# Optimization experiments

Measured on AMD Instinct MI355X. Metric: run time of the kernel, lower is better.

Reference implementation:

```python
import jax, jax.numpy as jnp
import numpy as np

B, N, H, D, N_HEADS = 8, 2048, 1024, 1, 8
SCALE = H / N_HEADS  # 128.0 ; note: NOT sqrt, faithful to source


def _linear(x, w, b):
    # torch nn.Linear: y = x @ W^T + b ; w: [out, in]
    return jnp.einsum('bnh,oh->bno', x, w) + b


def setup_inputs() -> dict:
    key = jax.random.key(0)
    ks = jax.random.split(key, 18)
    s = 0.02
    inp = {
        'node_t': jax.random.normal(ks[0], (B, N, H), dtype=jnp.float32),
        'node_next': jax.random.normal(ks[1], (B, N, H), dtype=jnp.float32),
        'WQ_w': s * jax.random.normal(ks[2], (H, H), dtype=jnp.float32),
        'WQ_b': s * jax.random.normal(ks[3], (H,), dtype=jnp.float32),
        'WK_w': s * jax.random.normal(ks[4], (H, H), dtype=jnp.float32),
        'WK_b': s * jax.random.normal(ks[5], (H,), dtype=jnp.float32),
        'WV_w': s * jax.random.normal(ks[6], (H, H), dtype=jnp.float32),
        'WV_b': s * jax.random.normal(ks[7], (H,), dtype=jnp.float32),
        'WO_w': s * jax.random.normal(ks[8], (H, H), dtype=jnp.float32),
        'WO_b': s * jax.random.normal(ks[9], (H,), dtype=jnp.float32),
        'WE_w': s * jax.random.normal(ks[10], (H, H), dtype=jnp.float32),
        'WE_b': s * jax.random.normal(ks[11], (H,), dtype=jnp.float32),
        'WN_w': s * jax.random.normal(ks[12], (H, H), dtype=jnp.float32),
        'WN_b': s * jax.random.normal(ks[13], (H,), dtype=jnp.float32),
        'WA_w': s * jax.random.normal(ks[14], (D, H), dtype=jnp.float32),
        'WA_b': s * jax.random.normal(ks[15], (D,), dtype=jnp.float32),
    }
    return inp


def reference(node_t, node_next, WQ_w, WQ_b, WK_w, WK_b, WV_w, WV_b,
              WO_w, WO_b, WE_w, WE_b, WN_w, WN_b, WA_w, WA_b):
    Q = _linear(node_t, WQ_w, WQ_b)       # [B,N,H]
    K = _linear(node_next, WK_w, WK_b)    # [B,N,H]
    V = _linear(node_next, WV_w, WV_b)    # [B,N,H]
    att = jnp.einsum('bih,bkh->bik', Q, K)  # [B,N,N]
    # torch nn.Softmax() with no dim on a 3-D tensor -> legacy dim=0 (batch axis)
    att = jax.nn.softmax(att / SCALE, axis=0)
    # einsum('bnn,bnd->bnd') uses only the diagonal att[b,n,n]
    diag = jnp.einsum('bnn->bn', att)  # [B,N]
    av = diag[:, :, None] * V          # [B,N,H]
    h = jax.nn.gelu(_linear(av, WO_w, WO_b), approximate=False)  # exact erf GELU
    A_t = _linear(node_t, WE_w, WE_b) + _linear(h, WN_w, WN_b)   # [B,N,H]
    A_t = _linear(A_t, WA_w, WA_b)     # [B,N,1]
    return jnp.squeeze(A_t, axis=-1)   # [B,N]
```

## Files before the change

### kernel.cpp

```cpp
#include <hip/hip_runtime.h>
#include <cstdint>
#include <cstddef>


typedef __attribute__((ext_vector_type(8))) short bfx8;
typedef __attribute__((ext_vector_type(4))) short s16x4;
typedef __attribute__((ext_vector_type(4))) float f32x4;

#define N_SEQ 2048
#define M_TOT 16384
#define NT 16

__device__ __forceinline__ unsigned short f2bf(float f) {
  unsigned int u = __float_as_uint(f);
  return (unsigned short)((u + 0x7fffu + ((u >> 16) & 1u)) >> 16);
}
__device__ __forceinline__ float bf2f(short s) {
  return __uint_as_float(((unsigned int)(unsigned short)s) << 16);
}
__device__ __forceinline__ float gelu_exact(float g) {
  return 0.5f * g * (1.0f + erff(g * 0.70710678118654752f));
}
__device__ __forceinline__ void gload16(const void* g, void* l) {
  __builtin_amdgcn_global_load_lds(
      (const __attribute__((address_space(1))) unsigned int*)g,
      (__attribute__((address_space(3))) unsigned int*)(unsigned int)(uintptr_t)l,
      16, 0, 0);
}
__device__ __forceinline__ float dot4(float4 a, float4 b) {
  return a.x * b.x + a.y * b.y + a.z * b.z + a.w * b.w;
}

__global__ __launch_bounds__(256) void prep_w(
    const float* __restrict__ WQ, const float* __restrict__ WK,
    const float* __restrict__ WV, const float* __restrict__ WO,
    const float* __restrict__ WE, const float* __restrict__ WN,
    const float* __restrict__ wa, const float* __restrict__ bQ,
    const float* __restrict__ bK, const float* __restrict__ bV,
    const float* __restrict__ WEb, const float* __restrict__ WNb,
    const float* __restrict__ WAb,
    short* __restrict__ wqT, short* __restrict__ wkT,
    short* __restrict__ wvT, short* __restrict__ wo_bf,
    float* __restrict__ vE, float* __restrict__ vN,
    float* __restrict__ uQ, float* __restrict__ uK,
    float* __restrict__ c0, float* __restrict__ c1,
    float* __restrict__ bvw) {
  __shared__ short tile[64][65];
  __shared__ float redw[4];
  int bid = blockIdx.x, t = threadIdx.x;
  if (bid < 1024) {
    int z = bid >> 8, idx = bid & 255, bi = idx >> 4, bj = idx & 15;
    const float* src = z == 0 ? WQ : z == 1 ? WK : z == 2 ? WV : WO;
    if (z == 3) {
#pragma unroll
      for (int i = 0; i < 16; ++i) {
        int lin = i * 256 + t, r = lin >> 6, c = lin & 63;
        size_t idx2 = (size_t)(bi * 64 + r) * 1024 + bj * 64 + c;
        wo_bf[idx2] = (short)f2bf(src[idx2]);
      }
      return;
    }
    short* dst = z == 0 ? wqT : z == 1 ? wkT : wvT;
#pragma unroll
    for (int i = 0; i < 16; ++i) {
      int lin = i * 256 + t, r = lin >> 6, c = lin & 63;
      tile[r][c] = (short)f2bf(src[(size_t)(bi * 64 + r) * 1024 + bj * 64 + c]);
    }
    __syncthreads();
#pragma unroll
    for (int i = 0; i < 16; ++i) {
      int lin = i * 256 + t, r = lin >> 6, c = lin & 63;
      dst[(size_t)(bj * 64 + r) * 1024 + bi * 64 + c] = tile[c][r];
    }
  } else if (bid < 1280) {
    int idx = bid - 1024;
    int y = idx >> 6, ob = idx & 63;
    const float* M = y == 0 ? WE : y == 1 ? WN : y == 2 ? WQ : WK;
    const float* wv = (y < 2) ? wa : (y == 2 ? bK : bQ);
    float* dst = y == 0 ? vE : y == 1 ? vN : y == 2 ? uQ : uK;
    float a0 = 0.f, a1 = 0.f, a2 = 0.f, a3 = 0.f;
    int o0 = ob * 16;
#pragma unroll
    for (int i = 0; i < 16; ++i) {
      int o = o0 + i;
      float wvv = wv[o];
      const float* row = M + (size_t)o * 1024;
      a0 += wvv * row[t];
      a1 += wvv * row[t + 256];
      a2 += wvv * row[t + 512];
      a3 += wvv * row[t + 768];
    }
    atomicAdd(dst + t, a0);
    atomicAdd(dst + t + 256, a1);
    atomicAdd(dst + t + 512, a2);
    atomicAdd(dst + t + 768, a3);
  } else if (bid < 1282) {
    int which = bid - 1280;
    float a = 0.f;
    if (which == 0)
      for (int i = t; i < 1024; i += 256) a += wa[i] * (WEb[i] + WNb[i]);
    else
      for (int i = t; i < 1024; i += 256) a += bQ[i] * bK[i];
#pragma unroll
    for (int o = 32; o > 0; o >>= 1) a += __shfl_down(a, o, 64);
    if ((t & 63) == 0) redw[t >> 6] = a;
    __syncthreads();
    if (t == 0) {
      float tot = redw[0] + redw[1] + redw[2] + redw[3];
      if (which == 0) c0[0] = tot + WAb[0];
      else c1[0] = tot;
    }
  } else {
    int r = bid - 1282;
    float4 wv = ((const float4*)(WO + (size_t)r * 1024))[t];
    float4 bv = ((const float4*)bV)[t];
    float a = dot4(wv, bv);
#pragma unroll
    for (int o = 32; o > 0; o >>= 1) a += __shfl_down(a, o, 64);
    if ((t & 63) == 0) redw[t >> 6] = a;
    __syncthreads();
    if (t == 0) bvw[r] = redw[0] + redw[1] + redw[2] + redw[3];
  }
}

__global__ __launch_bounds__(256) void prep2(
    const short* __restrict__ wqT, const short* __restrict__ wkT,
    const short* __restrict__ wvT, const short* __restrict__ wo_bf,
    short* __restrict__ M1, short* __restrict__ M2,
    const float* __restrict__ nn, const float* __restrict__ nt,
    const float* __restrict__ uK, const float* __restrict__ vE,
    short* __restrict__ xn, float* __restrict__ xk,
    float* __restrict__ xe) {
  __shared__ short sA[128 * 64];
  __shared__ short sB[128 * 64];
  int bid = blockIdx.x, tid = threadIdx.x;
  if (bid >= 128) {
    int lane = tid & 63, wv = tid >> 6;
    int isNT = bid >= 2176;
    int idx = bid - (isNT ? 2176 : 128);
    const float* srcm = isNT ? nt : nn;
    const float* vec = isNT ? vE : uK;
    const float4* v4 = (const float4*)vec + lane * 4;
    float4 u0 = v4[0], u1 = v4[1], u2 = v4[2], u3 = v4[3];
    int row = idx * 8 + wv * 2;
#pragma unroll
    for (int rr = 0; rr < 2; ++rr) {
      const float4* src = (const float4*)(srcm + (size_t)(row + rr) * 1024)
                          + lane * 4;
      float4 a0 = src[0], a1 = src[1], a2 = src[2], a3 = src[3];
      if (!isNT) {
        bfx8 o0, o1;
        o0[0] = (short)f2bf(a0.x); o0[1] = (short)f2bf(a0.y);
        o0[2] = (short)f2bf(a0.z); o0[3] = (short)f2bf(a0.w);
        o0[4] = (short)f2bf(a1.x); o0[5] = (short)f2bf(a1.y);
        o0[6] = (short)f2bf(a1.z); o0[7] = (short)f2bf(a1.w);
        o1[0] = (short)f2bf(a2.x); o1[1] = (short)f2bf(a2.y);
        o1[2] = (short)f2bf(a2.z); o1[3] = (short)f2bf(a2.w);
        o1[4] = (short)f2bf(a3.x); o1[5] = (short)f2bf(a3.y);
        o1[6] = (short)f2bf(a3.z); o1[7] = (short)f2bf(a3.w);
        bfx8* dst = (bfx8*)(xn + (size_t)(row + rr) * 1024 + lane * 16);
        dst[0] = o0; dst[1] = o1;
      }
      float a = dot4(a0, u0) + dot4(a1, u1) + dot4(a2, u2) + dot4(a3, u3);
#pragma unroll
      for (int o = 32; o > 0; o >>= 1) a += __shfl_xor(a, o, 64);
      if (lane == 0) (isNT ? xe : xk)[row + rr] = a;
    }
    return;
  }
  int z = bid >> 6, by = (bid >> 3) & 7, bx = bid & 7;
  const short* A = z ? wo_bf : wqT;
  const short* B = z ? wvT : wkT;
  short* D = z ? M2 : M1;
  int lane = tid & 63, w = tid >> 6;
  int wm = w >> 1, wn = w & 1;
  f32x4 acc[4][4] = {};
  int lrow = lane & 15, lk = (lane >> 4) * 8;
  int srow = lane >> 3, scol = (lane & 7) * 8;
  const short* Ag = A + (size_t)by * 128 * 1024;
  const short* Bg = B + (size_t)bx * 128 * 1024;
  for (int k0 = 0; k0 < 1024; k0 += 64) {
#pragma unroll
    for (int i = 0; i < 4; ++i) {
      int c = w * 4 + i;
      gload16(Ag + (size_t)(c * 8 + srow) * 1024 + k0 + scol, sA + c * 512);
      gload16(Bg + (size_t)(c * 8 + srow) * 1024 + k0 + scol, sB + c * 512);
    }
    __syncthreads();
#pragma unroll
    for (int kk = 0; kk < 64; kk += 32) {
      bfx8 af[4], bfr[4];
#pragma unroll
      for (int mi = 0; mi < 4; ++mi)
        af[mi] = *(const bfx8*)(sA + (wm * 64 + mi * 16 + lrow) * 64 + kk + lk);
#pragma unroll
      for (int nj = 0; nj < 4; ++nj)
        bfr[nj] = *(const bfx8*)(sB + (wn * 64 + nj * 16 + lrow) * 64 + kk + lk);
#pragma unroll
      for (int mi = 0; mi < 4; ++mi)
#pragma unroll
        for (int nj = 0; nj < 4; ++nj)
          acc[mi][nj] = __builtin_amdgcn_mfma_f32_16x16x32_bf16(
              af[mi], bfr[nj], acc[mi][nj], 0, 0, 0);
    }
    __syncthreads();
  }
  int r0 = by * 128 + wm * 64, cb2 = bx * 128 + wn * 64;
#pragma unroll
  for (int mi = 0; mi < 4; ++mi)
#pragma unroll
    for (int nj = 0; nj < 4; ++nj) {
      int col = cb2 + nj * 16 + lrow;
#pragma unroll
      for (int r = 0; r < 4; ++r) {
        int row = r0 + mi * 16 + (lane >> 4) * 4 + r;
        D[(size_t)row * 1024 + col] = (short)f2bf(acc[mi][nj][r]);
      }
    }
}

__global__ __launch_bounds__(256, 2) void gemm_main(
    const short* __restrict__ A, const short* __restrict__ Bf,
    const float* __restrict__ bias2, const float* __restrict__ nodet,
    float* __restrict__ sPart, short* __restrict__ vw) {
  __shared__ short sA[2][8192];
  __shared__ short sB[2][8192];
  int tid = threadIdx.x;
  int lane = tid & 63, w = tid >> 6;
  int wm = w >> 1, wn = w & 1;
  int wg = blockIdx.x;
  int work = (wg & 7) * 256 + (wg >> 3);
  int by = work >> 4, bx = work & 15;
  int lrow = lane & 15, g = lane >> 4;
  int sw0 = g ^ (lrow & 7);
  int sg = (lane & 7) ^ (lane >> 3);
  const short* Agt = A + ((size_t)(by * 128 + w * 32 + (lane >> 3))) * 1024 + sg * 8;
  const short* Bgt = Bf + ((size_t)(bx * 128 + w * 32 + (lane >> 3))) * 1024 + sg * 8;

  f32x4 acc[4][4] = {};

  auto stage = [&](int buf, int kt) {
    const short* ag = Agt + kt * 64;
    const short* bg = Bgt + kt * 64;
    short* la = &sA[buf][w * 2048];
    short* lb = &sB[buf][w * 2048];
#pragma unroll
    for (int i = 0; i < 4; ++i) {
      gload16(ag + i * 8192, la + i * 512);
      gload16(bg + i * 8192, lb + i * 512);
    }
  };

  stage(0, 0);
  int cur = 0;
  int arow = wm * 64 + lrow, brow = wn * 64 + lrow;
  for (int kt = 0; kt < NT; ++kt) {
    if (kt + 1 < NT) {
      stage(cur ^ 1, kt + 1);
      asm volatile("s_waitcnt vmcnt(8)" ::: "memory");
    } else {
      asm volatile("s_waitcnt vmcnt(0)" ::: "memory");
    }
    __builtin_amdgcn_sched_barrier(0);
    __builtin_amdgcn_s_barrier();
    __builtin_amdgcn_sched_barrier(0);

    const short* sa = &sA[cur][0];
    const short* sb = &sB[cur][0];
    bfx8 bq[4][2];
#pragma unroll
    for (int nj = 0; nj < 4; ++nj) {
      bq[nj][0] = *(const bfx8*)(sb + (brow + nj * 16) * 64 + sw0 * 8);
      bq[nj][1] = *(const bfx8*)(sb + (brow + nj * 16) * 64 + (sw0 ^ 4) * 8);
    }
#pragma unroll
    for (int q = 0; q < 2; ++q) {
      bfx8 a00 = *(const bfx8*)(sa + (arow + (2 * q) * 16) * 64 + sw0 * 8);
      bfx8 a01 = *(const bfx8*)(sa + (arow + (2 * q) * 16) * 64 + (sw0 ^ 4) * 8);
      bfx8 a10 = *(const bfx8*)(sa + (arow + (2 * q + 1) * 16) * 64 + sw0 * 8);
      bfx8 a11 = *(const bfx8*)(sa + (arow + (2 * q + 1) * 16) * 64 + (sw0 ^ 4) * 8);
      __builtin_amdgcn_s_setprio(1);
#pragma unroll
      for (int nj = 0; nj < 4; ++nj) {
        acc[2 * q][nj] = __builtin_amdgcn_mfma_f32_16x16x32_bf16(
            a00, bq[nj][0], acc[2 * q][nj], 0, 0, 0);
        acc[2 * q][nj] = __builtin_amdgcn_mfma_f32_16x16x32_bf16(
            a01, bq[nj][1], acc[2 * q][nj], 0, 0, 0);
        acc[2 * q + 1][nj] = __builtin_amdgcn_mfma_f32_16x16x32_bf16(
            a10, bq[nj][0], acc[2 * q + 1][nj], 0, 0, 0);
        acc[2 * q + 1][nj] = __builtin_amdgcn_mfma_f32_16x16x32_bf16(
            a11, bq[nj][1], acc[2 * q + 1][nj], 0, 0, 0);
      }
      __builtin_amdgcn_s_setprio(0);
    }
    __builtin_amdgcn_sched_barrier(0);
    __builtin_amdgcn_s_barrier();
    __builtin_amdgcn_sched_barrier(0);
    cur ^= 1;
  }

  int row0 = by * 128 + wm * 64;
  int cb = bx * 128 + wn * 64;
  if (bx < 8) {
    float bias_nj[4];
#pragma unroll
    for (int nj = 0; nj < 4; ++nj) bias_nj[nj] = bias2[cb + nj * 16 + lrow];
    int px = bx * 2 + wn;
#pragma unroll
    for (int mi = 0; mi < 4; ++mi) {
#pragma unroll
      for (int r = 0; r < 4; ++r) {
        int row = row0 + mi * 16 + g * 4 + r;
        const float* xr = nodet + (size_t)row * 1024;
        float v = 0.f;
#pragma unroll
        for (int nj = 0; nj < 4; ++nj)
          v += (acc[mi][nj][r] + bias_nj[nj]) * xr[cb + nj * 16 + lrow];
        v += __shfl_xor(v, 1, 64);
        v += __shfl_xor(v, 2, 64);
        v += __shfl_xor(v, 4, 64);
        v += __shfl_xor(v, 8, 64);
        if (lrow == 0) sPart[(size_t)row * 16 + px] = v;
      }
    }
  } else {
#pragma unroll
    for (int mi = 0; mi < 4; ++mi)
#pragma unroll
      for (int nj = 0; nj < 4; ++nj) {
        int colv = cb - 1024 + nj * 16 + lrow;
        float bv = bias2[1024 + colv];
#pragma unroll
        for (int r = 0; r < 4; ++r) {
          int row = row0 + mi * 16 + g * 4 + r;
          vw[(size_t)row * 1024 + colv] = (short)f2bf(acc[mi][nj][r] + bv);
        }
      }
  }
}

__global__ __launch_bounds__(512) void out2_kernel(
    const short* __restrict__ vw, const float* __restrict__ sPart,
    const float* __restrict__ xe, const float* __restrict__ xk,
    const float* __restrict__ vN, const float* __restrict__ bO,
    const float* __restrict__ c0p, const float* __restrict__ c1p,
    float* __restrict__ out) {
  int n = blockIdx.x, t = threadIdx.x;
  __shared__ float sS[8];
  if (t < 128) {
    int b = t >> 4, j = t & 15;
    size_t row = (size_t)b * N_SEQ + n;
    float p = sPart[row * 16 + j];
    p += __shfl_xor(p, 1, 64);
    p += __shfl_xor(p, 2, 64);
    p += __shfl_xor(p, 4, 64);
    p += __shfl_xor(p, 8, 64);
    if (j == 0) sS[b] = p + xk[row] + c1p[0];
  }
  __syncthreads();
  int b = t >> 6, lane = t & 63;
  float m = sS[0];
#pragma unroll
  for (int i = 1; i < 8; ++i) m = fmaxf(m, sS[i]);
  float sum = 0.f, eb = 0.f;
#pragma unroll
  for (int i = 0; i < 8; ++i) {
    float e = expf((sS[i] - m) * (1.0f / 128.0f));
    sum += e;
    if (i == b) eb = e;
  }
  float d = eb / sum;
  size_t row = (size_t)b * N_SEQ + n;
  const s16x4* vv = (const s16x4*)(vw + row * 1024 + lane * 16);
  const float4* bo4 = (const float4*)bO + lane * 4;
  const float4* vn4 = (const float4*)vN + lane * 4;
  float a = 0.f;
#pragma unroll
  for (int q = 0; q < 4; ++q) {
    s16x4 v = vv[q];
    float4 bo = bo4[q], vn = vn4[q];
    float gx;
    gx = fmaf(d, bf2f(v[0]), bo.x); a += gelu_exact(gx) * vn.x;
    gx = fmaf(d, bf2f(v[1]), bo.y); a += gelu_exact(gx) * vn.y;
    gx = fmaf(d, bf2f(v[2]), bo.z); a += gelu_exact(gx) * vn.z;
    gx = fmaf(d, bf2f(v[3]), bo.w); a += gelu_exact(gx) * vn.w;
  }
#pragma unroll
  for (int o = 32; o > 0; o >>= 1) a += __shfl_xor(a, o, 64);
  if (lane == 0) out[row] = xe[row] + c0p[0] + a;
}

extern "C" void kernel_launch(void* const* d_in, const int* in_sizes, int n_in,
                              void* d_out, int out_size, void* d_ws,
                              size_t ws_size, hipStream_t stream) {
  const float* nt  = (const float*)d_in[0];
  const float* nn  = (const float*)d_in[1];
  const float* WQ  = (const float*)d_in[2];
  const float* bQ  = (const float*)d_in[3];
  const float* WK  = (const float*)d_in[4];
  const float* bK  = (const float*)d_in[5];
  const float* WV  = (const float*)d_in[6];
  const float* bV  = (const float*)d_in[7];
  const float* WO  = (const float*)d_in[8];
  const float* bO  = (const float*)d_in[9];
  const float* WE  = (const float*)d_in[10];
  const float* WEb = (const float*)d_in[11];
  const float* WN  = (const float*)d_in[12];
  const float* WNb = (const float*)d_in[13];
  const float* wa  = (const float*)d_in[14];
  const float* WAb = (const float*)d_in[15];
  float* out = (float*)d_out;

  char* w = (char*)d_ws;
  size_t o = 0;
  const size_t BIG = (size_t)M_TOT * 1024 * 2;
  short* xn     = (short*)(w + o); o += BIG;
  short* vw     = (short*)(w + o); o += BIG;
  short* Bf     = (short*)(w + o); o += (size_t)2048 * 1024 * 2;
  short* wqT    = (short*)(w + o); o += 2097152;
  short* wkT    = (short*)(w + o); o += 2097152;
  short* wvT    = (short*)(w + o); o += 2097152;
  short* wo_bf  = (short*)(w + o); o += 2097152;
  float* sPart  = (float*)(w + o); o += (size_t)M_TOT * 16 * 4;
  float* bias2  = (float*)(w + o); o += 8192;
  float* vE     = (float*)(w + o); o += 4096;
  float* vN     = (float*)(w + o); o += 4096;
  float* uK     = (float*)(w + o); o += 4096;
  float* xk     = (float*)(w + o); o += 65536;
  float* xe     = (float*)(w + o); o += 65536;
  float* c0     = (float*)(w + o); o += 256;
  float* c1     = (float*)(w + o); o += 256;
  (void)ws_size; (void)in_sizes; (void)n_in; (void)out_size;

  hipMemsetAsync(bias2, 0, 8192 + 4096 * 3, stream);

  prep_w<<<2306, 256, 0, stream>>>(WQ, WK, WV, WO, WE, WN, wa, bQ, bK, bV,
                                   WEb, WNb, WAb, wqT, wkT, wvT, wo_bf,
                                   vE, vN, bias2, uK, c0, c1, bias2 + 1024);
  prep2<<<4224, 256, 0, stream>>>(wqT, wkT, wvT, wo_bf, Bf, Bf + 1048576,
                                  nn, nt, uK, vE, xn, xk, xe);
  gemm_main<<<2048, 256, 0, stream>>>(xn, Bf, bias2, nt, sPart, vw);
  out2_kernel<<<N_SEQ, 512, 0, stream>>>(vw, sPart, xe, xk, vN, bO,
                                         c0, c1, out);
}
```

Measured before the change: 152.9 us.

## Move node_t dot-product work into GEMM launch and retile block mapping

The node_t · vE row reductions move out of prep2 and into extra trailing blocks of gemm_main. This shortens the prep2 critical path, and the memory-bound reduction can fill GPU slots while or after the GEMM tiles run. The GEMM block-to-tile mapping also changes so each XCD handles 4x4 groups of tiles, which is meant to improve L2 reuse of A and B panels. The extra blocks add launch size to gemm_main and may compete for resources with the GEMM tail.

```diff
diff --git a/kernel.cpp b/kernel.cpp
--- a/kernel.cpp
+++ b/kernel.cpp
@@ -127,44 +127,37 @@
     const short* __restrict__ wqT, const short* __restrict__ wkT,
     const short* __restrict__ wvT, const short* __restrict__ wo_bf,
     short* __restrict__ M1, short* __restrict__ M2,
-    const float* __restrict__ nn, const float* __restrict__ nt,
-    const float* __restrict__ uK, const float* __restrict__ vE,
-    short* __restrict__ xn, float* __restrict__ xk,
-    float* __restrict__ xe) {
+    const float* __restrict__ nn, const float* __restrict__ uK,
+    short* __restrict__ xn, float* __restrict__ xk) {
   __shared__ short sA[128 * 64];
   __shared__ short sB[128 * 64];
   int bid = blockIdx.x, tid = threadIdx.x;
   if (bid >= 128) {
     int lane = tid & 63, wv = tid >> 6;
-    int isNT = bid >= 2176;
-    int idx = bid - (isNT ? 2176 : 128);
-    const float* srcm = isNT ? nt : nn;
-    const float* vec = isNT ? vE : uK;
-    const float4* v4 = (const float4*)vec + lane * 4;
+    int idx = bid - 128;
+    const float4* v4 = (const float4*)uK + lane * 4;
     float4 u0 = v4[0], u1 = v4[1], u2 = v4[2], u3 = v4[3];
     int row = idx * 8 + wv * 2;
 #pragma unroll
     for (int rr = 0; rr < 2; ++rr) {
-      const float4* src = (const float4*)(srcm + (size_t)(row + rr) * 1024)
+      const float4* src = (const float4*)(nn + (size_t)(row + rr) * 1024)
                           + lane * 4;
       float4 a0 = src[0], a1 = src[1], a2 = src[2], a3 = src[3];
-      if (!isNT) {
-        bfx8 o0, o1;
-        o0[0] = (short)f2bf(a0.x); o0[1] = (short)f2bf(a0.y);
-        o0[2] = (short)f2bf(a0.z); o0[3] = (short)f2bf(a0.w);
-        o0[4] = (short)f2bf(a1.x); o0[5] = (short)f2bf(a1.y);
-        o0[6] = (short)f2bf(a1.z); o0[7] = (short)f2bf(a1.w);
-        o1[0] = (short)f2bf(a2.x); o1[1] = (short)f2bf(a2.y);
-        o1[2] = (short)f2bf(a2.z); o1[3] = (short)f2bf(a2.w);
-        o1[4] = (short)f2bf(a3.x); o1[5] = (short)f2bf(a3.y);
-        o1[6] = (short)f2bf(a3.z); o1[7] = (short)f2bf(a3.w);
-        bfx8* dst = (bfx8*)(xn + (size_t)(row + rr) * 1024 + lane * 16);
-        dst[0] = o0; dst[1] = o1;
-      }
+      bfx8 o0, o1;
+      o0[0] = (short)f2bf(a0.x); o0[1] = (short)f2bf(a0.y);
+      o0[2] = (short)f2bf(a0.z); o0[3] = (short)f2bf(a0.w);
+      o0[4] = (short)f2bf(a1.x); o0[5] = (short)f2bf(a1.y);
+      o0[6] = (short)f2bf(a1.z); o0[7] = (short)f2bf(a1.w);
+      o1[0] = (short)f2bf(a2.x); o1[1] = (short)f2bf(a2.y);
+      o1[2] = (short)f2bf(a2.z); o1[3] = (short)f2bf(a2.w);
+      o1[4] = (short)f2bf(a3.x); o1[5] = (short)f2bf(a3.y);
+      o1[6] = (short)f2bf(a3.z); o1[7] = (short)f2bf(a3.w);
+      bfx8* dst = (bfx8*)(xn + (size_t)(row + rr) * 1024 + lane * 16);
+      dst[0] = o0; dst[1] = o1;
       float a = dot4(a0, u0) + dot4(a1, u1) + dot4(a2, u2) + dot4(a3, u3);
 #pragma unroll
       for (int o = 32; o > 0; o >>= 1) a += __shfl_xor(a, o, 64);
-      if (lane == 0) (isNT ? xe : xk)[row + rr] = a;
+      if (lane == 0) xk[row + rr] = a;
     }
     return;
   }
@@ -222,15 +215,36 @@
 __global__ __launch_bounds__(256, 2) void gemm_main(
     const short* __restrict__ A, const short* __restrict__ Bf,
     const float* __restrict__ bias2, const float* __restrict__ nodet,
+    const float* __restrict__ vE, float* __restrict__ xe,
     float* __restrict__ sPart, short* __restrict__ vw) {
   __shared__ short sA[2][8192];
   __shared__ short sB[2][8192];
   int tid = threadIdx.x;
+  if (blockIdx.x >= 2048) {
+    int lane = tid & 63, wv2 = tid >> 6;
+    int idx = blockIdx.x - 2048;
+    const float4* v4 = (const float4*)vE + lane * 4;
+    float4 u0 = v4[0], u1 = v4[1], u2 = v4[2], u3 = v4[3];
+    int row = idx * 8 + wv2 * 2;
+#pragma unroll
+    for (int rr = 0; rr < 2; ++rr) {
+      const float4* src = (const float4*)(nodet + (size_t)(row + rr) * 1024)
+                          + lane * 4;
+      float4 a0 = src[0], a1 = src[1], a2 = src[2], a3 = src[3];
+      float a = dot4(a0, u0) + dot4(a1, u1) + dot4(a2, u2) + dot4(a3, u3);
+#pragma unroll
+      for (int o = 32; o > 0; o >>= 1) a += __shfl_xor(a, o, 64);
+      if (lane == 0) xe[row + rr] = a;
+    }
+    return;
+  }
   int lane = tid & 63, w = tid >> 6;
   int wm = w >> 1, wn = w & 1;
   int wg = blockIdx.x;
-  int work = (wg & 7) * 256 + (wg >> 3);
-  int by = work >> 4, bx = work & 15;
+  int xcd = wg & 7, sub = wg >> 3;
+  int tt = sub >> 4, within = sub & 15;
+  int by = xcd * 16 + (tt >> 2) * 4 + (within >> 2);
+  int bx = (tt & 3) * 4 + (within & 3);
   int lrow = lane & 15, g = lane >> 4;
   int sw0 = g ^ (lrow & 7);
   int sg = (lane & 7) ^ (lane >> 3);
@@ -437,9 +451,9 @@
   prep_w<<<2306, 256, 0, stream>>>(WQ, WK, WV, WO, WE, WN, wa, bQ, bK, bV,
                                    WEb, WNb, WAb, wqT, wkT, wvT, wo_bf,
                                    vE, vN, bias2, uK, c0, c1, bias2 + 1024);
-  prep2<<<4224, 256, 0, stream>>>(wqT, wkT, wvT, wo_bf, Bf, Bf + 1048576,
-                                  nn, nt, uK, vE, xn, xk, xe);
-  gemm_main<<<2048, 256, 0, stream>>>(xn, Bf, bias2, nt, sPart, vw);
+  prep2<<<2176, 256, 0, stream>>>(wqT, wkT, wvT, wo_bf, Bf, Bf + 1048576,
+                                  nn, uK, xn, xk);
+  gemm_main<<<4096, 256, 0, stream>>>(xn, Bf, bias2, nt, vE, xe, sPart, vw);
   out2_kernel<<<N_SEQ, 512, 0, stream>>>(vw, sPart, xe, xk, vN, bO,
                                          c0, c1, out);
 }
```

After: 153.2 us. Within noise of the previous version (+0.2%).

## Drop double-buffered LDS in main GEMM for higher occupancy

Applied to the files above, without the earlier changes.

Replaces the double-buffered shared-memory staging in the main GEMM with a single buffer and raises the launch-bounds occupancy hint from 2 to 4 blocks per CU. Each k-step now loads, waits fully on vmcnt(0), then computes. This halves LDS use per block so more blocks can be resident, relying on inter-block concurrency to hide global latency instead of intra-block prefetch. The risk is exposed load latency per iteration and register pressure from the tighter launch bound.

```diff
diff --git a/kernel.cpp b/kernel.cpp
--- a/kernel.cpp
+++ b/kernel.cpp
@@ -219,12 +219,12 @@
     }
 }
 
-__global__ __launch_bounds__(256, 2) void gemm_main(
+__global__ __launch_bounds__(256, 4) void gemm_main(
     const short* __restrict__ A, const short* __restrict__ Bf,
     const float* __restrict__ bias2, const float* __restrict__ nodet,
     float* __restrict__ sPart, short* __restrict__ vw) {
-  __shared__ short sA[2][8192];
-  __shared__ short sB[2][8192];
+  __shared__ short sA[8192];
+  __shared__ short sB[8192];
   int tid = threadIdx.x;
   int lane = tid & 63, w = tid >> 6;
   int wm = w >> 1, wn = w & 1;
@@ -238,47 +238,35 @@
   const short* Bgt = Bf + ((size_t)(bx * 128 + w * 32 + (lane >> 3))) * 1024 + sg * 8;
 
   f32x4 acc[4][4] = {};
-
-  auto stage = [&](int buf, int kt) {
-    const short* ag = Agt + kt * 64;
-    const short* bg = Bgt + kt * 64;
-    short* la = &sA[buf][w * 2048];
-    short* lb = &sB[buf][w * 2048];
-#pragma unroll
-    for (int i = 0; i < 4; ++i) {
-      gload16(ag + i * 8192, la + i * 512);
-      gload16(bg + i * 8192, lb + i * 512);
-    }
-  };
-
-  stage(0, 0);
-  int cur = 0;
   int arow = wm * 64 + lrow, brow = wn * 64 + lrow;
+
   for (int kt = 0; kt < NT; ++kt) {
-    if (kt + 1 < NT) {
-      stage(cur ^ 1, kt + 1);
-      asm volatile("s_waitcnt vmcnt(8)" ::: "memory");
-    } else {
-      asm volatile("s_waitcnt vmcnt(0)" ::: "memory");
-    }
+    {
+      const short* ag = Agt + kt * 64;
+      const short* bg = Bgt + kt * 64;
+#pragma unroll
+      for (int i = 0; i < 4; ++i) {
+        gload16(ag + i * 8192, &sA[w * 2048 + i * 512]);
+        gload16(bg + i * 8192, &sB[w * 2048 + i * 512]);
+      }
+    }
+    asm volatile("s_waitcnt vmcnt(0)" ::: "memory");
     __builtin_amdgcn_sched_barrier(0);
     __builtin_amdgcn_s_barrier();
     __builtin_amdgcn_sched_barrier(0);
 
-    const short* sa = &sA[cur][0];
-    const short* sb = &sB[cur][0];
     bfx8 bq[4][2];
 #pragma unroll
     for (int nj = 0; nj < 4; ++nj) {
-      bq[nj][0] = *(const bfx8*)(sb + (brow + nj * 16) * 64 + sw0 * 8);
-      bq[nj][1] = *(const bfx8*)(sb + (brow + nj * 16) * 64 + (sw0 ^ 4) * 8);
+      bq[nj][0] = *(const bfx8*)(sB + (brow + nj * 16) * 64 + sw0 * 8);
+      bq[nj][1] = *(const bfx8*)(sB + (brow + nj * 16) * 64 + (sw0 ^ 4) * 8);
     }
 #pragma unroll
     for (int q = 0; q < 2; ++q) {
-      bfx8 a00 = *(const bfx8*)(sa + (arow + (2 * q) * 16) * 64 + sw0 * 8);
-      bfx8 a01 = *(const bfx8*)(sa + (arow + (2 * q) * 16) * 64 + (sw0 ^ 4) * 8);
-      bfx8 a10 = *(const bfx8*)(sa + (arow + (2 * q + 1) * 16) * 64 + sw0 * 8);
-      bfx8 a11 = *(const bfx8*)(sa + (arow + (2 * q + 1) * 16) * 64 + (sw0 ^ 4) * 8);
+      bfx8 a00 = *(const bfx8*)(sA + (arow + (2 * q) * 16) * 64 + sw0 * 8);
+      bfx8 a01 = *(const bfx8*)(sA + (arow + (2 * q) * 16) * 64 + (sw0 ^ 4) * 8);
+      bfx8 a10 = *(const bfx8*)(sA + (arow + (2 * q + 1) * 16) * 64 + sw0 * 8);
+      bfx8 a11 = *(const bfx8*)(sA + (arow + (2 * q + 1) * 16) * 64 + (sw0 ^ 4) * 8);
       __builtin_amdgcn_s_setprio(1);
 #pragma unroll
       for (int nj = 0; nj < 4; ++nj) {
@@ -296,7 +284,6 @@
     __builtin_amdgcn_sched_barrier(0);
     __builtin_amdgcn_s_barrier();
     __builtin_amdgcn_sched_barrier(0);
-    cur ^= 1;
   }
 
   int row0 = by * 128 + wm * 64;
```

Result: no change. 150.8 us (median of 3 runs) (-1.3%).
